# Optimization experiments

Hardware: AMD Instinct MI355X
Metric: run time of the kernel (lower is better)

## Reference

```python
import jax, jax.numpy as jnp
import numpy as np
from jax import lax

B, T, D = 4, 4096, 1024  # d_inner == D (expansion=1.0)


def setup_inputs() -> dict:
    key = jax.random.key(0)
    ks = jax.random.split(key, 6)
    s = 1.0 / np.sqrt(D)  # xavier-ish scale
    return {
        "x": jax.random.normal(ks[0], (B, T, D), dtype=jnp.float32),
        "W_in": jax.random.normal(ks[1], (D, D), dtype=jnp.float32) * s,
        "W_alpha": jax.random.normal(ks[2], (D, D), dtype=jnp.float32) * s,
        "b_alpha": jnp.full((D,), 2.0, dtype=jnp.float32),
        "W_beta": jax.random.normal(ks[3], (D, D), dtype=jnp.float32) * s,
        "b_beta": jnp.zeros((D,), dtype=jnp.float32),
        "W_v": jax.random.normal(ks[4], (D, D), dtype=jnp.float32) * s,
        "b_v": jnp.zeros((D,), dtype=jnp.float32),
        "W_out": jax.random.normal(ks[5], (D, D), dtype=jnp.float32) * s,
    }


def reference(x, W_in, W_alpha, b_alpha, W_beta, b_beta, W_v, b_v, W_out):
    # x: [B, T, D]; torch nn.Linear convention y = x @ W.T
    xp = jax.nn.silu(jnp.einsum("btd,ed->bte", x, W_in))  # [B, T, Di]
    alpha = jax.nn.sigmoid(jnp.einsum("bte,fe->btf", xp, W_alpha) + b_alpha)
    beta = jax.nn.sigmoid(jnp.einsum("bte,fe->btf", xp, W_beta) + b_beta)
    v = jnp.tanh(jnp.einsum("bte,fe->btf", xp, W_v) + b_v)
    bv = beta * v  # precompute write term

    def step(h, ab):
        a_t, bv_t = ab  # each [B, Di]
        h = a_t * h + bv_t
        return h, h * jax.nn.silu(h)

    h0 = jnp.zeros((x.shape[0], W_alpha.shape[0]), dtype=x.dtype)
    h_last, outs = lax.scan(step, h0, (alpha.transpose(1, 0, 2), bv.transpose(1, 0, 2)))
    cell_out = outs.transpose(1, 0, 2)  # [B, T, Di]
    output = jnp.einsum("btf,df->btd", cell_out, W_out)
    return output, h_last
```

## Files before the change

### kernel.cpp

```cpp
#include <hip/hip_runtime.h>
#include <hip/hip_bf16.h>
#include <cstdint>
#include <cstddef>

typedef __bf16 bf16_t;
typedef __bf16 bf16x8 __attribute__((ext_vector_type(8)));
typedef float  f32x4  __attribute__((ext_vector_type(4)));

constexpr int kBatch = 4;
constexpr int kT = 4096;
constexpr int kD = 1024;
constexpr int kM = kBatch * kT;
constexpr int kCH = kBatch * kD;
constexpr int kNC = 128;
constexpr int kL  = kT / kNC;
constexpr int LDS_BYTES = 131072;

__device__ __forceinline__ void async16(const bf16_t* g, char* l) {
    __builtin_amdgcn_global_load_lds(
        (const __attribute__((address_space(1))) uint32_t*)g,
        (__attribute__((address_space(3))) uint32_t*)l,
        16, 0, 0);
}

__global__ void cvt_bf16_kernel(const float* __restrict__ in, bf16_t* __restrict__ out, int n8) {
    int i = blockIdx.x * blockDim.x + threadIdx.x;
    if (i >= n8) return;
    const float4* p = reinterpret_cast<const float4*>(in) + 2 * (size_t)i;
    float4 a = p[0], b = p[1];
    bf16x8 o;
    o[0] = (bf16_t)a.x; o[1] = (bf16_t)a.y; o[2] = (bf16_t)a.z; o[3] = (bf16_t)a.w;
    o[4] = (bf16_t)b.x; o[5] = (bf16_t)b.y; o[6] = (bf16_t)b.z; o[7] = (bf16_t)b.w;
    *reinterpret_cast<bf16x8*>(out + 8 * (size_t)i) = o;
}

template<int EPI>
__global__ __launch_bounds__(512, 2)
void gemm256(const bf16_t* __restrict__ A, const bf16_t* __restrict__ Bw,
             const float* __restrict__ bias, const float* __restrict__ aux,
             void* __restrict__ outp, int M, int N, int K)
{
    extern __shared__ char lds[];
    const int tid  = threadIdx.x;
    const int lane = tid & 63;
    const int wv   = tid >> 6;
    const int wr   = wv >> 2;
    const int wc   = wv & 3;
    const int l16  = lane & 15;
    const int lhi  = lane >> 4;

    int bid = blockIdx.y * gridDim.x + blockIdx.x;
    int nwg = gridDim.x * gridDim.y;
    int swz = (bid & 7) * (nwg >> 3) + (bid >> 3);
    int gx  = N >> 8;
    int n0  = (swz % gx) << 8;
    int m0  = (swz / gx) << 8;

    auto goff = [&](int chunk) -> size_t {
        int st = chunk >> 6;
        int ri = (chunk >> 2) & 15;
        int cp = (chunk & 3) << 3;
        int cl = cp ^ (((ri >> 3) & 1) << 4);
        int gr = ((st >> 1) << 4) + ri;
        int gc = ((st & 1) << 5) + cl;
        return (size_t)gr * K + gc;
    };
    const size_t g0 = goff(tid), g1 = goff(512 + tid);
    const int d0 = wv << 10, d1 = 8192 + (wv << 10);

    auto STAGE = [&](const bf16_t* G, int row0, int k0, int lds_base) {
        const bf16_t* base = G + (size_t)row0 * K + k0;
        async16(base + g0, lds + lds_base + d0);
        async16(base + g1, lds + lds_base + d1);
    };

    auto ldsoff = [&](int r, int c) -> int {
        int ri = r & 15;
        int st = ((r >> 4) << 1) | (c >> 5);
        int cw = (c & 31) ^ (((ri >> 3) & 1) << 4);
        return (st << 10) + (ri << 6) + (cw << 1);
    };
    int offA[4][2], offB[2][2];
#pragma unroll
    for (int m = 0; m < 4; ++m)
#pragma unroll
        for (int s = 0; s < 2; ++s)
            offA[m][s] = ldsoff(wr * 64 + m * 16 + l16, s * 32 + lhi * 8);
#pragma unroll
    for (int n = 0; n < 2; ++n)
#pragma unroll
        for (int s = 0; s < 2; ++s)
            offB[n][s] = ldsoff(wc * 32 + n * 16 + l16, s * 32 + lhi * 8);

    f32x4 acc[8][4];
#pragma unroll
    for (int i = 0; i < 8; ++i)
#pragma unroll
        for (int j = 0; j < 4; ++j)
            acc[i][j] = (f32x4){0.f, 0.f, 0.f, 0.f};

    const int NT = K >> 6;

    STAGE(A,  m0,        0, 0);
    STAGE(A,  m0 + 128,  0, 16384);
    STAGE(Bw, n0,        0, 32768);
    STAGE(Bw, n0 + 128,  0, 49152);
    STAGE(A,  m0,       64, 65536);
    STAGE(Bw, n0 + 128, 64, 65536 + 49152);
    STAGE(A,  m0 + 128, 64, 65536 + 16384);
    asm volatile("s_waitcnt vmcnt(6)" ::: "memory");
    asm volatile("s_barrier" ::: "memory");

    for (int w = 0; w < NT; ++w) {
        const int bufo  = (w & 1) << 16;
        const int nbufo = bufo ^ 65536;
        const int oA0 = bufo, oA1 = bufo + 16384;
        const int oB0 = bufo + 32768, oB1 = bufo + 49152;
        const int k1 = (w + 1) << 6, k2 = (w + 2) << 6;
        bf16x8 aL[4][2], aH[4][2], bL[2][2], bH[2][2];

#pragma unroll
        for (int m = 0; m < 4; ++m)
#pragma unroll
            for (int s = 0; s < 2; ++s)
                aL[m][s] = *reinterpret_cast<const bf16x8*>(lds + oA0 + offA[m][s]);
#pragma unroll
        for (int n = 0; n < 2; ++n)
#pragma unroll
            for (int s = 0; s < 2; ++s)
                bL[n][s] = *reinterpret_cast<const bf16x8*>(lds + oB0 + offB[n][s]);
        if (w + 1 < NT) STAGE(Bw, n0, k1, nbufo + 32768);
        asm volatile("s_barrier" ::: "memory");
        __builtin_amdgcn_s_setprio(1);
#pragma unroll
        for (int m = 0; m < 4; ++m)
#pragma unroll
            for (int n = 0; n < 2; ++n)
#pragma unroll
                for (int s = 0; s < 2; ++s)
                    acc[m][n] = __builtin_amdgcn_mfma_f32_16x16x32_bf16(aL[m][s], bL[n][s], acc[m][n], 0, 0, 0);
        __builtin_amdgcn_s_setprio(0);
        asm volatile("s_barrier" ::: "memory");

#pragma unroll
        for (int n = 0; n < 2; ++n)
#pragma unroll
            for (int s = 0; s < 2; ++s)
                bH[n][s] = *reinterpret_cast<const bf16x8*>(lds + oB1 + offB[n][s]);
        if (w + 2 < NT) STAGE(A, m0, k2, oA0);
        asm volatile("s_barrier" ::: "memory");
        __builtin_amdgcn_s_setprio(1);
#pragma unroll
        for (int m = 0; m < 4; ++m)
#pragma unroll
            for (int n = 0; n < 2; ++n)
#pragma unroll
                for (int s = 0; s < 2; ++s)
                    acc[m][2 + n] = __builtin_amdgcn_mfma_f32_16x16x32_bf16(aL[m][s], bH[n][s], acc[m][2 + n], 0, 0, 0);
        __builtin_amdgcn_s_setprio(0);
        asm volatile("s_barrier" ::: "memory");

#pragma unroll
        for (int m = 0; m < 4; ++m)
#pragma unroll
            for (int s = 0; s < 2; ++s)
                aH[m][s] = *reinterpret_cast<const bf16x8*>(lds + oA1 + offA[m][s]);
        if (w + 2 < NT) STAGE(Bw, n0 + 128, k2, oB1);
        asm volatile("s_barrier" ::: "memory");
        __builtin_amdgcn_s_setprio(1);
#pragma unroll
        for (int m = 0; m < 4; ++m)
#pragma unroll
            for (int n = 0; n < 2; ++n)
#pragma unroll
                for (int s = 0; s < 2; ++s)
                    acc[4 + m][n] = __builtin_amdgcn_mfma_f32_16x16x32_bf16(aH[m][s], bL[n][s], acc[4 + m][n], 0, 0, 0);
        __builtin_amdgcn_s_setprio(0);
        asm volatile("s_barrier" ::: "memory");

        if (w + 2 < NT) STAGE(A, m0 + 128, k2, oA1);
        asm volatile("s_barrier" ::: "memory");
        __builtin_amdgcn_s_setprio(1);
#pragma unroll
        for (int m = 0; m < 4; ++m)
#pragma unroll
            for (int n = 0; n < 2; ++n)
#pragma unroll
                for (int s = 0; s < 2; ++s)
                    acc[4 + m][2 + n] = __builtin_amdgcn_mfma_f32_16x16x32_bf16(aH[m][s], bH[n][s], acc[4 + m][2 + n], 0, 0, 0);
        __builtin_amdgcn_s_setprio(0);
        if (w + 2 < NT) {
            asm volatile("s_waitcnt vmcnt(6)" ::: "memory");
        } else if (w + 2 == NT) {
            asm volatile("s_waitcnt vmcnt(0)" ::: "memory");
        }
        if (w + 1 < NT) asm volatile("s_barrier" ::: "memory");
    }

#pragma unroll
    for (int j = 0; j < 4; ++j) {
        const int colg = n0 + ((j >> 1) << 7) + wc * 32 + (j & 1) * 16 + l16;
        float bs = 0.f;
        if constexpr (EPI == 1 || EPI == 2) bs = bias[colg];
#pragma unroll
        for (int i = 0; i < 8; ++i) {
            const int rb = m0 + ((i >> 2) << 7) + wr * 64 + (i & 3) * 16 + lhi * 4;
#pragma unroll
            for (int r = 0; r < 4; ++r) {
                const size_t idx = (size_t)(rb + r) * N + colg;
                const float f = acc[i][j][r];
                if constexpr (EPI == 0) {
                    float s = f / (1.f + __expf(-f));
                    reinterpret_cast<bf16_t*>(outp)[idx] = (bf16_t)s;
                } else if constexpr (EPI == 1) {
                    reinterpret_cast<float*>(outp)[idx] = 1.f / (1.f + __expf(-(f + bs)));
                } else if constexpr (EPI == 2) {
                    reinterpret_cast<float*>(outp)[idx] = aux[idx] * tanhf(f + bs);
                } else {
                    reinterpret_cast<float*>(outp)[idx] = f;
                }
            }
        }
    }
}

__global__ void scan_chunk_kernel(const float* __restrict__ alpha,
                                  const float* __restrict__ bv,
                                  float* __restrict__ Aagg,
                                  float* __restrict__ Bagg)
{
    const int u  = blockIdx.x * blockDim.x + threadIdx.x;
    const int ch = u & (kCH - 1);
    const int c  = u >> 12;
    const int b  = ch >> 10;
    const int d  = ch & (kD - 1);
    size_t base = ((size_t)b * kT + (size_t)c * kL) * kD + d;
    float Ac = 1.f, Bc = 0.f;
#pragma unroll 4
    for (int t = 0; t < kL; ++t) {
        float a = alpha[base];
        float v = bv[base];
        Ac *= a;
        Bc = a * Bc + v;
        base += kD;
    }
    Aagg[u] = Ac;
    Bagg[u] = Bc;
}

__global__ void scan_mid_kernel(const float* __restrict__ Aagg,
                                const float* __restrict__ Bagg,
                                float* __restrict__ Hin,
                                float* __restrict__ hlast)
{
    const int ch = blockIdx.x * blockDim.x + threadIdx.x;
    float h = 0.f;
#pragma unroll 8
    for (int c = 0; c < kNC; ++c) {
        Hin[(size_t)c * kCH + ch] = h;
        h = Aagg[(size_t)c * kCH + ch] * h + Bagg[(size_t)c * kCH + ch];
    }
    hlast[ch] = h;
}

__global__ void scan_out_kernel(const float* __restrict__ alpha,
                                const float* __restrict__ bv,
                                const float* __restrict__ Hin,
                                bf16_t* __restrict__ cell)
{
    const int u  = blockIdx.x * blockDim.x + threadIdx.x;
    const int ch = u & (kCH - 1);
    const int c  = u >> 12;
    const int b  = ch >> 10;
    const int d  = ch & (kD - 1);
    size_t base = ((size_t)b * kT + (size_t)c * kL) * kD + d;
    float h = Hin[u];
#pragma unroll 4
    for (int t = 0; t < kL; ++t) {
        float a = alpha[base];
        float v = bv[base];
        h = a * h + v;
        float s = 1.f / (1.f + __expf(-h));
        cell[base] = (bf16_t)(h * h * s);
        base += kD;
    }
}

extern "C" void kernel_launch(void* const* d_in, const int* in_sizes, int n_in,
                              void* d_out, int out_size, void* d_ws, size_t ws_size,
                              hipStream_t stream)
{
    const float* x     = (const float*)d_in[0];
    const float* W_in  = (const float*)d_in[1];
    const float* W_al  = (const float*)d_in[2];
    const float* b_al  = (const float*)d_in[3];
    const float* W_be  = (const float*)d_in[4];
    const float* b_be  = (const float*)d_in[5];
    const float* W_v   = (const float*)d_in[6];
    const float* b_v   = (const float*)d_in[7];
    const float* W_out = (const float*)d_in[8];

    float* out   = (float*)d_out;
    float* hlast = out + (size_t)kM * kD;

    char* ws = (char*)d_ws;
    size_t off = 0;
    auto alloc = [&](size_t bytes) -> void* {
        void* p = ws + off;
        off += (bytes + 255) & ~(size_t)255;
        return p;
    };
    bf16_t* xbf   = (bf16_t*)alloc((size_t)kM * kD * 2);
    bf16_t* xp    = (bf16_t*)alloc((size_t)kM * kD * 2);
    float*  alpha = (float*) alloc((size_t)kM * kD * 4);
    float*  bvb   = (float*) alloc((size_t)kM * kD * 4);
    bf16_t* wbf   = (bf16_t*)alloc((size_t)5 * kD * kD * 2);

    bf16_t* Winb = wbf;
    bf16_t* Walb = wbf + 1 * (size_t)kD * kD;
    bf16_t* Wbeb = wbf + 2 * (size_t)kD * kD;
    bf16_t* Wvb  = wbf + 3 * (size_t)kD * kD;
    bf16_t* Wob  = wbf + 4 * (size_t)kD * kD;

    bf16_t* cell = xbf;
    float*  Aagg = (float*)xp;
    float*  Bagg = Aagg + (size_t)kNC * kCH;
    float*  Hin  = Bagg + (size_t)kNC * kCH;

    hipFuncSetAttribute(reinterpret_cast<const void*>(gemm256<0>), hipFuncAttributeMaxDynamicSharedMemorySize, LDS_BYTES);
    hipFuncSetAttribute(reinterpret_cast<const void*>(gemm256<1>), hipFuncAttributeMaxDynamicSharedMemorySize, LDS_BYTES);
    hipFuncSetAttribute(reinterpret_cast<const void*>(gemm256<2>), hipFuncAttributeMaxDynamicSharedMemorySize, LDS_BYTES);
    hipFuncSetAttribute(reinterpret_cast<const void*>(gemm256<3>), hipFuncAttributeMaxDynamicSharedMemorySize, LDS_BYTES);

    {
        int n8 = kM * kD / 8;
        cvt_bf16_kernel<<<(n8 + 255) / 256, 256, 0, stream>>>(x, xbf, n8);
        int w8 = kD * kD / 8;
        int wg = (w8 + 255) / 256;
        cvt_bf16_kernel<<<wg, 256, 0, stream>>>(W_in,  Winb, w8);
        cvt_bf16_kernel<<<wg, 256, 0, stream>>>(W_al,  Walb, w8);
        cvt_bf16_kernel<<<wg, 256, 0, stream>>>(W_be,  Wbeb, w8);
        cvt_bf16_kernel<<<wg, 256, 0, stream>>>(W_v,   Wvb,  w8);
        cvt_bf16_kernel<<<wg, 256, 0, stream>>>(W_out, Wob,  w8);
    }

    dim3 grid(kD / 256, kM / 256);

    gemm256<0><<<grid, 512, LDS_BYTES, stream>>>(xbf, Winb, nullptr, nullptr, xp, kM, kD, kD);
    gemm256<1><<<grid, 512, LDS_BYTES, stream>>>(xp, Walb, b_al, nullptr, alpha, kM, kD, kD);
    gemm256<1><<<grid, 512, LDS_BYTES, stream>>>(xp, Wbeb, b_be, nullptr, bvb, kM, kD, kD);
    gemm256<2><<<grid, 512, LDS_BYTES, stream>>>(xp, Wvb, b_v, bvb, bvb, kM, kD, kD);

    scan_chunk_kernel<<<kNC * kCH / 256, 256, 0, stream>>>(alpha, bvb, Aagg, Bagg);
    scan_mid_kernel<<<kCH / 256, 256, 0, stream>>>(Aagg, Bagg, Hin, hlast);
    scan_out_kernel<<<kNC * kCH / 256, 256, 0, stream>>>(alpha, bvb, Hin, cell);

    gemm256<3><<<grid, 512, LDS_BYTES, stream>>>(cell, Wob, nullptr, nullptr, out, kM, kD, kD);
}
```

Baseline: 349.4 us.

## Fuse alpha/beta/v projections into one wide GEMM with bf16 beta and v outputs

The three projections from xp are merged into one GEMM with N=3*D over the contiguous converted weights. Each 1024-column slab picks its own bias and epilogue. Beta and v are now written as separate bf16 arrays, and the scan kernels form beta*v on the fly. This removes the reread of the fp32 bv buffer in the v epilogue and two GEMM launches. The five weight conversions become one launch, and outputs use nontemporal stores. The scan now reads two bf16 arrays instead of one fp32 array, so its traffic stays the same, and beta*v is computed from bf16-rounded factors, which costs some precision.

```diff
diff --git a/kernel.cpp b/kernel.cpp
--- a/kernel.cpp
+++ b/kernel.cpp
@@ -34,11 +34,28 @@
     *reinterpret_cast<bf16x8*>(out + 8 * (size_t)i) = o;
 }
 
+__global__ void cvtw_kernel(const float* __restrict__ w0, const float* __restrict__ w1,
+                            const float* __restrict__ w2, const float* __restrict__ w3,
+                            const float* __restrict__ w4, bf16_t* __restrict__ out) {
+    const int per = kD * kD / 8;
+    int i = blockIdx.x * blockDim.x + threadIdx.x;
+    int seg = i / per, j = i - seg * per;
+    const float* src = seg == 0 ? w0 : seg == 1 ? w1 : seg == 2 ? w2 : seg == 3 ? w3 : w4;
+    const float4* p = reinterpret_cast<const float4*>(src) + 2 * (size_t)j;
+    float4 a = p[0], b = p[1];
+    bf16x8 o;
+    o[0] = (bf16_t)a.x; o[1] = (bf16_t)a.y; o[2] = (bf16_t)a.z; o[3] = (bf16_t)a.w;
+    o[4] = (bf16_t)b.x; o[5] = (bf16_t)b.y; o[6] = (bf16_t)b.z; o[7] = (bf16_t)b.w;
+    *reinterpret_cast<bf16x8*>(out + ((size_t)seg * per + j) * 8) = o;
+}
+
 template<int EPI>
 __global__ __launch_bounds__(512, 2)
 void gemm256(const bf16_t* __restrict__ A, const bf16_t* __restrict__ Bw,
-             const float* __restrict__ bias, const float* __restrict__ aux,
-             void* __restrict__ outp, int M, int N, int K)
+             const float* __restrict__ bi0, const float* __restrict__ bi1,
+             const float* __restrict__ bi2,
+             void* __restrict__ out0, void* __restrict__ out1, void* __restrict__ out2,
+             int M, int N, int K)
 {
     extern __shared__ char lds[];
     const int tid  = threadIdx.x;
@@ -197,27 +214,38 @@
         if (w + 1 < NT) asm volatile("s_barrier" ::: "memory");
     }
 
+    const int slab = n0 >> 10;
+    const float* bia = (EPI == 4) ? (slab == 0 ? bi0 : slab == 1 ? bi1 : bi2) : nullptr;
 #pragma unroll
     for (int j = 0; j < 4; ++j) {
         const int colg = n0 + ((j >> 1) << 7) + wc * 32 + (j & 1) * 16 + l16;
+        const int cL = colg & (kD - 1);
         float bs = 0.f;
-        if constexpr (EPI == 1 || EPI == 2) bs = bias[colg];
+        if constexpr (EPI == 4) bs = bia[cL];
 #pragma unroll
         for (int i = 0; i < 8; ++i) {
             const int rb = m0 + ((i >> 2) << 7) + wr * 64 + (i & 3) * 16 + lhi * 4;
 #pragma unroll
             for (int r = 0; r < 4; ++r) {
-                const size_t idx = (size_t)(rb + r) * N + colg;
+                const int rowg = rb + r;
                 const float f = acc[i][j][r];
                 if constexpr (EPI == 0) {
                     float s = f / (1.f + __expf(-f));
-                    reinterpret_cast<bf16_t*>(outp)[idx] = (bf16_t)s;
-                } else if constexpr (EPI == 1) {
-                    reinterpret_cast<float*>(outp)[idx] = 1.f / (1.f + __expf(-(f + bs)));
-                } else if constexpr (EPI == 2) {
-                    reinterpret_cast<float*>(outp)[idx] = aux[idx] * tanhf(f + bs);
+                    reinterpret_cast<bf16_t*>(out0)[(size_t)rowg * N + colg] = (bf16_t)s;
+                } else if constexpr (EPI == 3) {
+                    __builtin_nontemporal_store(f, reinterpret_cast<float*>(out0) + (size_t)rowg * N + colg);
                 } else {
-                    reinterpret_cast<float*>(outp)[idx] = f;
+                    const size_t idx = (size_t)rowg * kD + cL;
+                    if (slab == 0) {
+                        float s = 1.f / (1.f + __expf(-(f + bs)));
+                        __builtin_nontemporal_store(s, reinterpret_cast<float*>(out0) + idx);
+                    } else if (slab == 1) {
+                        float s = 1.f / (1.f + __expf(-(f + bs)));
+                        __builtin_nontemporal_store((bf16_t)s, reinterpret_cast<bf16_t*>(out1) + idx);
+                    } else {
+                        float s = tanhf(f + bs);
+                        __builtin_nontemporal_store((bf16_t)s, reinterpret_cast<bf16_t*>(out2) + idx);
+                    }
                 }
             }
         }
@@ -225,7 +253,8 @@
 }
 
 __global__ void scan_chunk_kernel(const float* __restrict__ alpha,
-                                  const float* __restrict__ bv,
+                                  const bf16_t* __restrict__ beta,
+                                  const bf16_t* __restrict__ vv,
                                   float* __restrict__ Aagg,
                                   float* __restrict__ Bagg)
 {
@@ -238,10 +267,10 @@
     float Ac = 1.f, Bc = 0.f;
 #pragma unroll 4
     for (int t = 0; t < kL; ++t) {
-        float a = alpha[base];
-        float v = bv[base];
+        float a  = alpha[base];
+        float bv = (float)beta[base] * (float)vv[base];
         Ac *= a;
-        Bc = a * Bc + v;
+        Bc = a * Bc + bv;
         base += kD;
     }
     Aagg[u] = Ac;
@@ -264,7 +293,8 @@
 }
 
 __global__ void scan_out_kernel(const float* __restrict__ alpha,
-                                const float* __restrict__ bv,
+                                const bf16_t* __restrict__ beta,
+                                const bf16_t* __restrict__ vv,
                                 const float* __restrict__ Hin,
                                 bf16_t* __restrict__ cell)
 {
@@ -277,9 +307,9 @@
     float h = Hin[u];
 #pragma unroll 4
     for (int t = 0; t < kL; ++t) {
-        float a = alpha[base];
-        float v = bv[base];
-        h = a * h + v;
+        float a  = alpha[base];
+        float bv = (float)beta[base] * (float)vv[base];
+        h = a * h + bv;
         float s = 1.f / (1.f + __expf(-h));
         cell[base] = (bf16_t)(h * h * s);
         base += kD;
@@ -313,13 +343,12 @@
     bf16_t* xbf   = (bf16_t*)alloc((size_t)kM * kD * 2);
     bf16_t* xp    = (bf16_t*)alloc((size_t)kM * kD * 2);
     float*  alpha = (float*) alloc((size_t)kM * kD * 4);
-    float*  bvb   = (float*) alloc((size_t)kM * kD * 4);
+    bf16_t* betab = (bf16_t*)alloc((size_t)kM * kD * 2);
+    bf16_t* vb    = (bf16_t*)alloc((size_t)kM * kD * 2);
     bf16_t* wbf   = (bf16_t*)alloc((size_t)5 * kD * kD * 2);
 
     bf16_t* Winb = wbf;
-    bf16_t* Walb = wbf + 1 * (size_t)kD * kD;
-    bf16_t* Wbeb = wbf + 2 * (size_t)kD * kD;
-    bf16_t* Wvb  = wbf + 3 * (size_t)kD * kD;
+    bf16_t* Wfus = wbf + 1 * (size_t)kD * kD;
     bf16_t* Wob  = wbf + 4 * (size_t)kD * kD;
 
     bf16_t* cell = xbf;
@@ -328,32 +357,27 @@
     float*  Hin  = Bagg + (size_t)kNC * kCH;
 
     hipFuncSetAttribute(reinterpret_cast<const void*>(gemm256<0>), hipFuncAttributeMaxDynamicSharedMemorySize, LDS_BYTES);
-    hipFuncSetAttribute(reinterpret_cast<const void*>(gemm256<1>), hipFuncAttributeMaxDynamicSharedMemorySize, LDS_BYTES);
-    hipFuncSetAttribute(reinterpret_cast<const void*>(gemm256<2>), hipFuncAttributeMaxDynamicSharedMemorySize, LDS_BYTES);
     hipFuncSetAttribute(reinterpret_cast<const void*>(gemm256<3>), hipFuncAttributeMaxDynamicSharedMemorySize, LDS_BYTES);
+    hipFuncSetAttribute(reinterpret_cast<const void*>(gemm256<4>), hipFuncAttributeMaxDynamicSharedMemorySize, LDS_BYTES);
 
     {
         int n8 = kM * kD / 8;
         cvt_bf16_kernel<<<(n8 + 255) / 256, 256, 0, stream>>>(x, xbf, n8);
-        int w8 = kD * kD / 8;
-        int wg = (w8 + 255) / 256;
-        cvt_bf16_kernel<<<wg, 256, 0, stream>>>(W_in,  Winb, w8);
-        cvt_bf16_kernel<<<wg, 256, 0, stream>>>(W_al,  Walb, w8);
-        cvt_bf16_kernel<<<wg, 256, 0, stream>>>(W_be,  Wbeb, w8);
-        cvt_bf16_kernel<<<wg, 256, 0, stream>>>(W_v,   Wvb,  w8);
-        cvt_bf16_kernel<<<wg, 256, 0, stream>>>(W_out, Wob,  w8);
-    }
-
-    dim3 grid(kD / 256, kM / 256);
-
-    gemm256<0><<<grid, 512, LDS_BYTES, stream>>>(xbf, Winb, nullptr, nullptr, xp, kM, kD, kD);
-    gemm256<1><<<grid, 512, LDS_BYTES, stream>>>(xp, Walb, b_al, nullptr, alpha, kM, kD, kD);
-    gemm256<1><<<grid, 512, LDS_BYTES, stream>>>(xp, Wbeb, b_be, nullptr, bvb, kM, kD, kD);
-    gemm256<2><<<grid, 512, LDS_BYTES, stream>>>(xp, Wvb, b_v, bvb, bvb, kM, kD, kD);
-
-    scan_chunk_kernel<<<kNC * kCH / 256, 256, 0, stream>>>(alpha, bvb, Aagg, Bagg);
+        int wtot = 5 * kD * kD / 8;
+        cvtw_kernel<<<(wtot + 255) / 256, 256, 0, stream>>>(W_in, W_al, W_be, W_v, W_out, wbf);
+    }
+
+    dim3 grid1(kD / 256, kM / 256);
+    dim3 gridF(3 * kD / 256, kM / 256);
+
+    gemm256<0><<<grid1, 512, LDS_BYTES, stream>>>(xbf, Winb, nullptr, nullptr, nullptr,
+                                                  xp, nullptr, nullptr, kM, kD, kD);
+    gemm256<4><<<gridF, 512, LDS_BYTES, stream>>>(xp, Wfus, b_al, b_be, b_v,
+                                                  alpha, betab, vb, kM, 3 * kD, kD);
+    scan_chunk_kernel<<<kNC * kCH / 256, 256, 0, stream>>>(alpha, betab, vb, Aagg, Bagg);
     scan_mid_kernel<<<kCH / 256, 256, 0, stream>>>(Aagg, Bagg, Hin, hlast);
-    scan_out_kernel<<<kNC * kCH / 256, 256, 0, stream>>>(alpha, bvb, Hin, cell);
-
-    gemm256<3><<<grid, 512, LDS_BYTES, stream>>>(cell, Wob, nullptr, nullptr, out, kM, kD, kD);
-}
+    scan_out_kernel<<<kNC * kCH / 256, 256, 0, stream>>>(alpha, betab, vb, Hin, cell);
+
+    gemm256<3><<<grid1, 512, LDS_BYTES, stream>>>(cell, Wob, nullptr, nullptr, nullptr,
+                                                  out, nullptr, nullptr, kM, kD, kD);
+}
```

Result: no change. 347.2 us (-0.6%).
